# Kernel optimization log

Hardware: AMD Instinct MI355X
Metric: run time of the kernel (lower is better)

## Reference

```python
import jax, jax.numpy as jnp
import numpy as np

M, N, D = 16384, 16384, 256


def setup_inputs() -> dict:
    key = jax.random.key(0)
    k1, k2, k3 = jax.random.split(key, 3)
    x = jax.random.normal(k1, (M, D), dtype=jnp.float32)
    X = jax.random.normal(k2, (N, D), dtype=jnp.float32)
    residuals = jax.random.normal(k3, (N,), dtype=jnp.float32)
    return {"x": x, "X": X, "residuals": residuals}


def reference(x, X, residuals):
    n, d = X.shape
    # Scott's rule: h = mean(std(X, unbiased)) * n^(-1/(d+4))
    h = jnp.mean(jnp.std(X, axis=0, ddof=1)) * (n ** (-1.0 / (d + 4)))
    inv_bw_sq = 1.0 / (2.0 * h * h)
    sq = (jnp.sum(x * x, axis=1)[:, None]
          + jnp.sum(X * X, axis=1)[None, :]
          - 2.0 * (x @ X.T))
    sq = jnp.maximum(sq, 0.0)
    w = jnp.exp(-sq * inv_bw_sq)                     # (m, n)
    num = w @ residuals                              # (m,)
    den = jnp.sum(w, axis=1) + 1e-8                  # (m,)
    return num / den
```

## Files before the change

kernel.cpp:

```cpp
#include <hip/hip_runtime.h>
#include <stdint.h>

#define MDIM 16384
#define NDIM 16384
#define DDIM 256
#define NSPLIT 4
#define NSTRIP 4096
#define BM 128
#define NT 32

typedef __attribute__((ext_vector_type(16))) float f32x16;
typedef __attribute__((ext_vector_type(8))) int i32x8;

#define SC1 0x7F7F7F7F

static constexpr size_t COLPART_OFF = 0;
static constexpr size_t SCAL_OFF    = 512u * 1024u;
static constexpr size_t AX_OFF      = SCAL_OFF + 1024u;
static constexpr size_t BXR_OFF     = AX_OFF + 64u * 1024u;
static constexpr size_t BXM_OFF     = BXR_OFF + 64u * 1024u;
static constexpr size_t X8_OFF      = 1ull << 20;
static constexpr size_t B8_OFF      = X8_OFF + (4ull << 20);
static constexpr size_t NUMP_OFF    = B8_OFF + (4ull << 20) + (512ull << 10);
static constexpr size_t DENP_OFF    = NUMP_OFF + (size_t)NSPLIT * MDIM * 4u;

__device__ inline unsigned short f2bf_rne(float f) {
    uint32_t u = __builtin_bit_cast(uint32_t, f);
    u += 0x7fffu + ((u >> 16) & 1u);
    return (unsigned short)(u >> 16);
}

__global__ void k1_colstats(const float* __restrict__ X, float2* __restrict__ part) {
    const int l  = threadIdx.x & 63;
    const int wv = threadIdx.x >> 6;
    const int b  = blockIdx.x;
    const float* p = X + (size_t)(b * 256 + wv * 64) * DDIM + l * 4;
    float4 s = {0.f, 0.f, 0.f, 0.f}, q = {0.f, 0.f, 0.f, 0.f};
#pragma unroll 8
    for (int r = 0; r < 64; ++r) {
        float4 v = *(const float4*)(p + (size_t)r * DDIM);
        s.x += v.x; s.y += v.y; s.z += v.z; s.w += v.w;
        q.x += v.x * v.x; q.y += v.y * v.y; q.z += v.z * v.z; q.w += v.w * v.w;
    }
    __shared__ float4 sA[4][64], qA[4][64];
    sA[wv][l] = s; qA[wv][l] = q;
    __syncthreads();
    if (wv == 0) {
#pragma unroll
        for (int i = 1; i < 4; ++i) {
            float4 si = sA[i][l], qi = qA[i][l];
            s.x += si.x; s.y += si.y; s.z += si.z; s.w += si.w;
            q.x += qi.x; q.y += qi.y; q.z += qi.z; q.w += qi.w;
        }
        part[b * 256 + l * 4 + 0] = make_float2(s.x, q.x);
        part[b * 256 + l * 4 + 1] = make_float2(s.y, q.y);
        part[b * 256 + l * 4 + 2] = make_float2(s.z, q.z);
        part[b * 256 + l * 4 + 3] = make_float2(s.w, q.w);
    }
}

__global__ void k2_finalize(const float2* __restrict__ part, float* __restrict__ scal) {
    const int t = threadIdx.x;
    float s = 0.f, sq = 0.f;
#pragma unroll 8
    for (int b = 0; b < 64; ++b) {
        float2 v = part[b * 256 + t];
        s += v.x; sq += v.y;
    }
    const float n = (float)NDIM;
    float var = (sq - s * s / n) / (n - 1.0f);
    float sd  = sqrtf(fmaxf(var, 0.f));
    __shared__ float red[256];
    red[t] = sd;
    __syncthreads();
    for (int o = 128; o > 0; o >>= 1) {
        if (t < o) red[t] += red[t + o];
        __syncthreads();
    }
    if (t == 0) {
        float h = (red[0] / 256.0f) * exp2f(log2f(n) * (-1.0f / (DDIM + 4.0f)));
        float c = 1.0f / (2.0f * h * h);
        scal[0] = c;
        scal[1] = sqrtf(2.0f * c);
    }
}

__global__ void k3_prep(const float* __restrict__ x, const float* __restrict__ X,
                        unsigned char* __restrict__ x8T, unsigned char* __restrict__ B8T,
                        float* __restrict__ ax,
                        const float* __restrict__ resid, unsigned int* __restrict__ bxrp,
                        unsigned int* __restrict__ bxminu,
                        const float* __restrict__ scal) {
    const int l    = threadIdx.x & 63;
    const int wv   = threadIdx.x >> 6;
    const bool isB = blockIdx.x >= (MDIM / 16);
    const int row  = (blockIdx.x - (isB ? MDIM / 16 : 0)) * 16 + wv * 4 + (l >> 4);
    const int q    = l & 15;
    const float* src = isB ? X : x;
    const float c = scal[0], s = scal[1];

    float4 v[4];
    const float* pr = src + (size_t)row * DDIM + q * 16;
#pragma unroll
    for (int i = 0; i < 4; ++i) v[i] = *(const float4*)(pr + i * 4);

    float nsq = 0.f;
#pragma unroll
    for (int i = 0; i < 4; ++i)
        nsq += v[i].x * v[i].x + v[i].y * v[i].y + v[i].z * v[i].z + v[i].w * v[i].w;
#pragma unroll
    for (int o = 1; o < 16; o <<= 1) nsq += __shfl_xor(nsq, o);

    uint4 u;
    {
        unsigned int t0 = 0, t1 = 0, t2 = 0, t3 = 0;
        t0 = __builtin_amdgcn_cvt_pk_fp8_f32(v[0].x * s, v[0].y * s, t0, 0);
        t0 = __builtin_amdgcn_cvt_pk_fp8_f32(v[0].z * s, v[0].w * s, t0, 1);
        t1 = __builtin_amdgcn_cvt_pk_fp8_f32(v[1].x * s, v[1].y * s, t1, 0);
        t1 = __builtin_amdgcn_cvt_pk_fp8_f32(v[1].z * s, v[1].w * s, t1, 1);
        t2 = __builtin_amdgcn_cvt_pk_fp8_f32(v[2].x * s, v[2].y * s, t2, 0);
        t2 = __builtin_amdgcn_cvt_pk_fp8_f32(v[2].z * s, v[2].w * s, t2, 1);
        t3 = __builtin_amdgcn_cvt_pk_fp8_f32(v[3].x * s, v[3].y * s, t3, 0);
        t3 = __builtin_amdgcn_cvt_pk_fp8_f32(v[3].z * s, v[3].w * s, t3, 1);
        u = make_uint4(t0, t1, t2, t3);
    }

    const int ks64 = q >> 2, lh = (q >> 1) & 1, eh = q & 1;
    if (isB) {
        const size_t off = (size_t)(row >> 6) * 16384 + ks64 * 4096 + ((row >> 5) & 1) * 2048
                         + lh * 1024 + (row & 31) * 32 + eh * 16;
        *(uint4*)(B8T + off) = u;
        if (q == 0) {
            bxrp[row] = ((unsigned int)f2bf_rne(resid[row]) << 16) | f2bf_rne(-c * nsq);
            atomicMin(&bxminu[row >> 6], __builtin_bit_cast(unsigned int, nsq));
        }
    } else {
        const size_t off = (size_t)(row >> 7) * 32768 + ks64 * 8192 + ((row >> 5) & 3) * 2048
                         + lh * 1024 + (row & 31) * 32 + eh * 16;
        *(uint4*)(x8T + off) = u;
        if (q == 0) ax[row] = -c * nsq;
    }
}

__global__ __launch_bounds__(256, 2)
void k4_main(const unsigned char* __restrict__ x8T, const unsigned char* __restrict__ B8T,
             const float* __restrict__ ax, const unsigned int* __restrict__ bxrp,
             const unsigned int* __restrict__ bxminu, const float* __restrict__ scal,
             float* __restrict__ nump, float* __restrict__ denp) {
    __shared__ float ldsBxm[NSTRIP / 64];
    __shared__ float ldsAcc[2 * BM];

    const int tid  = threadIdx.x;
    const int lane = tid & 63;
    const int wv   = tid >> 6;
    const int wr   = wv >> 1;
    const int wc   = wv & 1;
    const int l31  = lane & 31;
    const int lhi  = lane >> 5;

    const int f  = blockIdx.x;
    const int sw = (f & 7) * 64 + (f >> 3);
    const int mt = sw & 127;
    const int by = sw >> 7;
    const int m0 = mt * BM;
    const int n0 = by * NSTRIP;

    const float c = scal[0];
    if (tid < NSTRIP / 64)
        ldsBxm[tid] = -c * __builtin_bit_cast(float, bxminu[(n0 >> 6) + tid]);
    ldsAcc[tid] = 0.f;

    float axm = fmaxf(ax[m0 + lane], ax[m0 + 64 + lane]);
#pragma unroll
    for (int o = 1; o < 64; o <<= 1) axm = fmaxf(axm, __shfl_xor(axm, o));

    const unsigned char* Ab = x8T + (size_t)mt * 32768 + lhi * 1024 + l31 * 32;
    i32x8 aF[2][4];
#pragma unroll
    for (int rf = 0; rf < 2; ++rf)
#pragma unroll
        for (int ks = 0; ks < 4; ++ks)
            aF[rf][ks] = *(const i32x8*)(Ab + ks * 8192 + (wr * 2 + rf) * 2048);

    const unsigned char* Bb = B8T + (size_t)n0 * 256 + (size_t)wc * 16384 + lhi * 1024 + l31 * 32;
    i32x8 bF[4][2];
#pragma unroll
    for (int s = 0; s < 2; ++s) {
        bF[s][0] = *(const i32x8*)(Bb + s * 4096);
        bF[s][1] = *(const i32x8*)(Bb + s * 4096 + 2048);
    }

    __syncthreads();

    if ((f >> 8) & 1) __builtin_amdgcn_s_sleep(4);

    f32x16 acc[2][2];

#pragma unroll 1
    for (int nt = 0; nt < NT; ++nt) {
#pragma unroll
        for (int ks = 0; ks < 4; ++ks) {
            {
                const int sp = nt * 4 + ks + 2;
                const size_t off = (size_t)(sp >> 2) * 32768 + (size_t)(sp & 3) * 4096;
                bF[(ks + 2) & 3][0] = *(const i32x8*)(Bb + off);
                bF[(ks + 2) & 3][1] = *(const i32x8*)(Bb + off + 2048);
            }
            __builtin_amdgcn_sched_barrier(0);
            __builtin_amdgcn_s_setprio(1);
#pragma unroll
            for (int rf = 0; rf < 2; ++rf)
#pragma unroll
                for (int cf = 0; cf < 2; ++cf) {
                    if (ks == 0)
                        acc[rf][cf] = __builtin_amdgcn_mfma_scale_f32_32x32x64_f8f6f4(
                            aF[rf][ks], bF[ks & 3][cf], (f32x16)(0.f), 0, 0, 0, SC1, 0, SC1);
                    else
                        acc[rf][cf] = __builtin_amdgcn_mfma_scale_f32_32x32x64_f8f6f4(
                            aF[rf][ks], bF[ks & 3][cf], acc[rf][cf], 0, 0, 0, SC1, 0, SC1);
                }
            __builtin_amdgcn_s_setprio(0);
            __builtin_amdgcn_sched_barrier(0);

            if (ks == 3) {
                const float bxm = ldsBxm[nt * 2 + wc];
                float m = -1e30f;
#pragma unroll
                for (int i = 0; i < 2; ++i)
#pragma unroll
                    for (int j = 0; j < 2; ++j)
#pragma unroll
                        for (int r = 0; r < 16; r += 4) {
                            f32x16 v = acc[i][j];
                            m = fmaxf(m, fmaxf(fmaxf(v[r], v[r + 1]), fmaxf(v[r + 2], v[r + 3])));
                        }
                if (!__all(m + axm + bxm < -104.0f)) {
                    float bxv[2], rv[2];
#pragma unroll
                    for (int cf = 0; cf < 2; ++cf) {
                        unsigned int pk = bxrp[n0 + nt * 128 + wc * 64 + cf * 32 + l31];
                        bxv[cf] = __builtin_bit_cast(float, pk << 16);
                        rv[cf]  = __builtin_bit_cast(float, pk & 0xffff0000u);
                    }
#pragma unroll
                    for (int rf = 0; rf < 2; ++rf)
#pragma unroll
                        for (int r = 0; r < 16; ++r) {
                            const int row = wr * 64 + rf * 32 + (r & 3) + 8 * (r >> 2) + 4 * lhi;
                            const float axv = ax[m0 + row];
                            float nv = 0.f, dv = 0.f;
#pragma unroll
                            for (int cf = 0; cf < 2; ++cf) {
                                const float arg = fminf(acc[rf][cf][r] + axv + bxv[cf], 0.f);
                                const float w = expf(arg);
                                nv = fmaf(w, rv[cf], nv);
                                dv += w;
                            }
#pragma unroll
                            for (int o = 1; o < 32; o <<= 1) { nv += __shfl_xor(nv, o); dv += __shfl_xor(dv, o); }
                            if (l31 == 0) {
                                atomicAdd(&ldsAcc[row * 2 + 0], nv);
                                atomicAdd(&ldsAcc[row * 2 + 1], dv);
                            }
                        }
                }
            }
        }
    }

    __syncthreads();
    if (tid < BM) {
        nump[by * MDIM + m0 + tid] = ldsAcc[tid * 2 + 0];
        denp[by * MDIM + m0 + tid] = ldsAcc[tid * 2 + 1];
    }
}

__global__ void k5_div(const float* __restrict__ nump, const float* __restrict__ denp,
                       float* __restrict__ out) {
    const int i = blockIdx.x * 256 + threadIdx.x;
    float n = 0.f, d = 0.f;
#pragma unroll
    for (int s = 0; s < NSPLIT; ++s) { n += nump[s * MDIM + i]; d += denp[s * MDIM + i]; }
    out[i] = n / (d + 1e-8f);
}

extern "C" void kernel_launch(void* const* d_in, const int* in_sizes, int n_in,
                              void* d_out, int out_size, void* d_ws, size_t ws_size,
                              hipStream_t stream) {
    const float* x     = (const float*)d_in[0];
    const float* X     = (const float*)d_in[1];
    const float* resid = (const float*)d_in[2];
    float* out = (float*)d_out;

    char* w = (char*)d_ws;
    float2* colpart      = (float2*)(w + COLPART_OFF);
    float*  scal         = (float*)(w + SCAL_OFF);
    float*  ax           = (float*)(w + AX_OFF);
    unsigned int* bxrp   = (unsigned int*)(w + BXR_OFF);
    unsigned int* bxminu = (unsigned int*)(w + BXM_OFF);
    unsigned char* x8    = (unsigned char*)(w + X8_OFF);
    unsigned char* B8    = (unsigned char*)(w + B8_OFF);
    float* nump          = (float*)(w + NUMP_OFF);
    float* denp          = (float*)(w + DENP_OFF);

    k1_colstats<<<64, 256, 0, stream>>>(X, colpart);
    k2_finalize<<<1, 256, 0, stream>>>(colpart, scal);
    k3_prep<<<(MDIM + NDIM) / 16, 256, 0, stream>>>(x, X, x8, B8, ax, resid, bxrp, bxminu, scal);
    k4_main<<<512, 256, 0, stream>>>(x8, B8, ax, bxrp, bxminu, scal, nump, denp);
    k5_div<<<MDIM / 256, 256, 0, stream>>>(nump, denp, out);
}
```

Before: 95.77 us.

## Stage B tiles through LDS with async global_load_lds instead of per-wave register loads

Changes the B8 packing layout to 16-byte rows and streams B fragments into a 4-slot LDS ring buffer with direct global-to-LDS loads. The waves now share one copy of each B tile instead of each wave loading its own fragments into registers. Synchronisation uses explicit vmcnt waits and a workgroup barrier every k-step, and the staggered s_sleep is removed. This is meant to cut redundant global traffic and register pressure, but it adds a barrier per MFMA group plus LDS read latency.

```diff
diff --git a/kernel.cpp b/kernel.cpp
--- a/kernel.cpp
+++ b/kernel.cpp
@@ -11,6 +11,7 @@
 
 typedef __attribute__((ext_vector_type(16))) float f32x16;
 typedef __attribute__((ext_vector_type(8))) int i32x8;
+typedef __attribute__((ext_vector_type(4))) int i32x4;
 
 #define SC1 0x7F7F7F7F
 
@@ -28,6 +29,11 @@
     uint32_t u = __builtin_bit_cast(uint32_t, f);
     u += 0x7fffu + ((u >> 16) & 1u);
     return (unsigned short)(u >> 16);
+}
+
+__device__ inline void gload16(const void* g, void* l) {
+    __builtin_amdgcn_global_load_lds((const __attribute__((address_space(1))) void*)g,
+                                     (__attribute__((address_space(3))) void*)l, 16, 0, 0);
 }
 
 __global__ void k1_colstats(const float* __restrict__ X, float2* __restrict__ part) {
@@ -127,8 +133,8 @@
 
     const int ks64 = q >> 2, lh = (q >> 1) & 1, eh = q & 1;
     if (isB) {
-        const size_t off = (size_t)(row >> 6) * 16384 + ks64 * 4096 + ((row >> 5) & 1) * 2048
-                         + lh * 1024 + (row & 31) * 32 + eh * 16;
+        const size_t off = (size_t)(row >> 6) * 16384 + ks64 * 4096 + eh * 2048
+                         + lh * 1024 + (row & 63) * 16;
         *(uint4*)(B8T + off) = u;
         if (q == 0) {
             bxrp[row] = ((unsigned int)f2bf_rne(resid[row]) << 16) | f2bf_rne(-c * nsq);
@@ -147,6 +153,7 @@
              const float* __restrict__ ax, const unsigned int* __restrict__ bxrp,
              const unsigned int* __restrict__ bxminu, const float* __restrict__ scal,
              float* __restrict__ nump, float* __restrict__ denp) {
+    __shared__ unsigned char ldsB[4 * 8192];
     __shared__ float ldsBxm[NSTRIP / 64];
     __shared__ float ldsAcc[2 * BM];
 
@@ -166,13 +173,8 @@
     const int n0 = by * NSTRIP;
 
     const float c = scal[0];
-    if (tid < NSTRIP / 64)
-        ldsBxm[tid] = -c * __builtin_bit_cast(float, bxminu[(n0 >> 6) + tid]);
-    ldsAcc[tid] = 0.f;
-
-    float axm = fmaxf(ax[m0 + lane], ax[m0 + 64 + lane]);
-#pragma unroll
-    for (int o = 1; o < 64; o <<= 1) axm = fmaxf(axm, __shfl_xor(axm, o));
+    const float ax0 = ax[m0 + lane], ax1 = ax[m0 + 64 + lane];
+    const float bxmv = -c * __builtin_bit_cast(float, bxminu[(n0 >> 6) + lane]);
 
     const unsigned char* Ab = x8T + (size_t)mt * 32768 + lhi * 1024 + l31 * 32;
     i32x8 aF[2][4];
@@ -182,48 +184,70 @@
         for (int ks = 0; ks < 4; ++ks)
             aF[rf][ks] = *(const i32x8*)(Ab + ks * 8192 + (wr * 2 + rf) * 2048);
 
-    const unsigned char* Bb = B8T + (size_t)n0 * 256 + (size_t)wc * 16384 + lhi * 1024 + l31 * 32;
-    i32x8 bF[4][2];
-#pragma unroll
-    for (int s = 0; s < 2; ++s) {
-        bF[s][0] = *(const i32x8*)(Bb + s * 4096);
-        bF[s][1] = *(const i32x8*)(Bb + s * 4096 + 2048);
-    }
-
-    __syncthreads();
-
-    if ((f >> 8) & 1) __builtin_amdgcn_s_sleep(4);
+    if (wv == 0) ldsBxm[lane] = bxmv;
+    ldsAcc[tid] = 0.f;
+
+    float axm = fmaxf(ax0, ax1);
+#pragma unroll
+    for (int o = 1; o < 64; o <<= 1) axm = fmaxf(axm, __shfl_xor(axm, o));
+
+    asm volatile("s_waitcnt vmcnt(0) lgkmcnt(0)" ::: "memory");
+    __builtin_amdgcn_sched_barrier(0);
+    __builtin_amdgcn_s_barrier();
+
+    auto stage = [&](int step) {
+        const int t    = (step >> 2) & (NT - 1);
+        const int ks64 = step & 3;
+        const int slot = step & 3;
+        const unsigned char* src = B8T + (size_t)((n0 >> 6) + t * 2 + wc) * 16384
+                                 + ks64 * 4096 + wr * 1024 + lane * 16;
+        char* dst = (char*)ldsB + slot * 8192 + wc * 4096 + wr * 1024;
+        gload16(src, dst);
+        gload16(src + 2048, dst + 2048);
+    };
+    auto ldb = [&](int step, int cf) -> i32x8 {
+        const unsigned char* p = ldsB + (step & 3) * 8192 + wc * 4096
+                               + lhi * 1024 + (cf * 32 + l31) * 16;
+        i32x4 lo = *(const i32x4*)p;
+        i32x4 hi = *(const i32x4*)(p + 2048);
+        return (i32x8){lo[0], lo[1], lo[2], lo[3], hi[0], hi[1], hi[2], hi[3]};
+    };
+
+    stage(0); stage(1);
 
     f32x16 acc[2][2];
 
 #pragma unroll 1
-    for (int nt = 0; nt < NT; ++nt) {
+    for (int nt_ = 0; nt_ < NT; ++nt_) {
 #pragma unroll
         for (int ks = 0; ks < 4; ++ks) {
-            {
-                const int sp = nt * 4 + ks + 2;
-                const size_t off = (size_t)(sp >> 2) * 32768 + (size_t)(sp & 3) * 4096;
-                bF[(ks + 2) & 3][0] = *(const i32x8*)(Bb + off);
-                bF[(ks + 2) & 3][1] = *(const i32x8*)(Bb + off + 2048);
+            const int s = nt_ * 4 + ks;
+            stage(s + 2);
+            asm volatile("s_waitcnt vmcnt(4)" ::: "memory");
+            __builtin_amdgcn_sched_barrier(0);
+            __builtin_amdgcn_s_barrier();
+            i32x8 b0 = ldb(s, 0);
+            i32x8 b1 = ldb(s, 1);
+            __builtin_amdgcn_s_setprio(1);
+#pragma unroll
+            for (int rf = 0; rf < 2; ++rf) {
+                if (ks == 0) {
+                    acc[rf][0] = __builtin_amdgcn_mfma_scale_f32_32x32x64_f8f6f4(
+                        aF[rf][ks], b0, (f32x16)(0.f), 0, 0, 0, SC1, 0, SC1);
+                    acc[rf][1] = __builtin_amdgcn_mfma_scale_f32_32x32x64_f8f6f4(
+                        aF[rf][ks], b1, (f32x16)(0.f), 0, 0, 0, SC1, 0, SC1);
+                } else {
+                    acc[rf][0] = __builtin_amdgcn_mfma_scale_f32_32x32x64_f8f6f4(
+                        aF[rf][ks], b0, acc[rf][0], 0, 0, 0, SC1, 0, SC1);
+                    acc[rf][1] = __builtin_amdgcn_mfma_scale_f32_32x32x64_f8f6f4(
+                        aF[rf][ks], b1, acc[rf][1], 0, 0, 0, SC1, 0, SC1);
+                }
             }
-            __builtin_amdgcn_sched_barrier(0);
-            __builtin_amdgcn_s_setprio(1);
-#pragma unroll
-            for (int rf = 0; rf < 2; ++rf)
-#pragma unroll
-                for (int cf = 0; cf < 2; ++cf) {
-                    if (ks == 0)
-                        acc[rf][cf] = __builtin_amdgcn_mfma_scale_f32_32x32x64_f8f6f4(
-                            aF[rf][ks], bF[ks & 3][cf], (f32x16)(0.f), 0, 0, 0, SC1, 0, SC1);
-                    else
-                        acc[rf][cf] = __builtin_amdgcn_mfma_scale_f32_32x32x64_f8f6f4(
-                            aF[rf][ks], bF[ks & 3][cf], acc[rf][cf], 0, 0, 0, SC1, 0, SC1);
-                }
             __builtin_amdgcn_s_setprio(0);
             __builtin_amdgcn_sched_barrier(0);
 
             if (ks == 3) {
-                const float bxm = ldsBxm[nt * 2 + wc];
+                const float bxm = ldsBxm[nt_ * 2 + wc];
                 float m = -1e30f;
 #pragma unroll
                 for (int i = 0; i < 2; ++i)
@@ -238,7 +262,7 @@
                     float bxv[2], rv[2];
 #pragma unroll
                     for (int cf = 0; cf < 2; ++cf) {
-                        unsigned int pk = bxrp[n0 + nt * 128 + wc * 64 + cf * 32 + l31];
+                        unsigned int pk = bxrp[n0 + nt_ * 128 + wc * 64 + cf * 32 + l31];
                         bxv[cf] = __builtin_bit_cast(float, pk << 16);
                         rv[cf]  = __builtin_bit_cast(float, pk & 0xffff0000u);
                     }
@@ -263,11 +287,14 @@
                                 atomicAdd(&ldsAcc[row * 2 + 1], dv);
                             }
                         }
+                    asm volatile("s_waitcnt vmcnt(0)" ::: "memory");
                 }
             }
         }
     }
 
+    asm volatile("s_waitcnt vmcnt(0) lgkmcnt(0)" ::: "memory");
+    __builtin_amdgcn_sched_barrier(0);
     __syncthreads();
     if (tid < BM) {
         nump[by * MDIM + m0 + tid] = ldsAcc[tid * 2 + 0];
```

After: 100.5 us. 1.05x slower.

## Quantize operands to FP4 e2m1 and use FP4 scaled MFMA

Applied to the files above, without the earlier changes.

Switches the packed x and X operands from FP8 to FP4 (e2m1) with a custom threshold quantizer. Memory layouts are repacked at half the bytes, and the scaled MFMA is run in FP4 mode with the upper half of each operand register zeroed. This halves operand bandwidth and may raise MFMA throughput, at a large accuracy cost for the distance computation inside an exponential. It also drops the staggered s_sleep for half of the blocks.

```diff
diff --git a/kernel.cpp b/kernel.cpp
--- a/kernel.cpp
+++ b/kernel.cpp
@@ -11,6 +11,7 @@
 
 typedef __attribute__((ext_vector_type(16))) float f32x16;
 typedef __attribute__((ext_vector_type(8))) int i32x8;
+typedef __attribute__((ext_vector_type(4))) int i32x4;
 
 #define SC1 0x7F7F7F7F
 
@@ -28,6 +29,14 @@
     uint32_t u = __builtin_bit_cast(uint32_t, f);
     u += 0x7fffu + ((u >> 16) & 1u);
     return (unsigned short)(u >> 16);
+}
+
+__device__ inline unsigned e2m1q(float v) {
+    const float a = __builtin_fabsf(v);
+    unsigned m = (unsigned)(a >= 0.25f) + (unsigned)(a >= 0.75f) + (unsigned)(a >= 1.25f)
+               + (unsigned)(a >= 1.75f) + (unsigned)(a >= 2.5f)  + (unsigned)(a >= 3.5f)
+               + (unsigned)(a >= 5.0f);
+    return m | ((__builtin_bit_cast(unsigned, v) >> 28) & 8u);
 }
 
 __global__ void k1_colstats(const float* __restrict__ X, float2* __restrict__ part) {
@@ -111,33 +120,31 @@
 #pragma unroll
     for (int o = 1; o < 16; o <<= 1) nsq += __shfl_xor(nsq, o);
 
-    uint4 u;
-    {
-        unsigned int t0 = 0, t1 = 0, t2 = 0, t3 = 0;
-        t0 = __builtin_amdgcn_cvt_pk_fp8_f32(v[0].x * s, v[0].y * s, t0, 0);
-        t0 = __builtin_amdgcn_cvt_pk_fp8_f32(v[0].z * s, v[0].w * s, t0, 1);
-        t1 = __builtin_amdgcn_cvt_pk_fp8_f32(v[1].x * s, v[1].y * s, t1, 0);
-        t1 = __builtin_amdgcn_cvt_pk_fp8_f32(v[1].z * s, v[1].w * s, t1, 1);
-        t2 = __builtin_amdgcn_cvt_pk_fp8_f32(v[2].x * s, v[2].y * s, t2, 0);
-        t2 = __builtin_amdgcn_cvt_pk_fp8_f32(v[2].z * s, v[2].w * s, t2, 1);
-        t3 = __builtin_amdgcn_cvt_pk_fp8_f32(v[3].x * s, v[3].y * s, t3, 0);
-        t3 = __builtin_amdgcn_cvt_pk_fp8_f32(v[3].z * s, v[3].w * s, t3, 1);
-        u = make_uint4(t0, t1, t2, t3);
-    }
-
-    const int ks64 = q >> 2, lh = (q >> 1) & 1, eh = q & 1;
+    float vs[16] = {v[0].x * s, v[0].y * s, v[0].z * s, v[0].w * s,
+                    v[1].x * s, v[1].y * s, v[1].z * s, v[1].w * s,
+                    v[2].x * s, v[2].y * s, v[2].z * s, v[2].w * s,
+                    v[3].x * s, v[3].y * s, v[3].z * s, v[3].w * s};
+    unsigned w0 = 0, w1 = 0;
+#pragma unroll
+    for (int i = 0; i < 4; ++i) {
+        w0 |= (e2m1q(vs[2 * i]) | (e2m1q(vs[2 * i + 1]) << 4)) << (8 * i);
+        w1 |= (e2m1q(vs[8 + 2 * i]) | (e2m1q(vs[9 + 2 * i]) << 4)) << (8 * i);
+    }
+    const uint2 u = make_uint2(w0, w1);
+
+    const int ks64 = q >> 2, lh = (q >> 1) & 1, eb = q & 1;
     if (isB) {
-        const size_t off = (size_t)(row >> 6) * 16384 + ks64 * 4096 + ((row >> 5) & 1) * 2048
-                         + lh * 1024 + (row & 31) * 32 + eh * 16;
-        *(uint4*)(B8T + off) = u;
+        const size_t off = (size_t)(row >> 6) * 8192 + ks64 * 2048 + lh * 1024
+                         + (row & 63) * 16 + eb * 8;
+        *(uint2*)(B8T + off) = u;
         if (q == 0) {
             bxrp[row] = ((unsigned int)f2bf_rne(resid[row]) << 16) | f2bf_rne(-c * nsq);
             atomicMin(&bxminu[row >> 6], __builtin_bit_cast(unsigned int, nsq));
         }
     } else {
-        const size_t off = (size_t)(row >> 7) * 32768 + ks64 * 8192 + ((row >> 5) & 3) * 2048
-                         + lh * 1024 + (row & 31) * 32 + eh * 16;
-        *(uint4*)(x8T + off) = u;
+        const size_t off = (size_t)(row >> 7) * 16384 + ks64 * 4096 + ((row >> 5) & 3) * 1024
+                         + lh * 512 + (row & 31) * 16 + eb * 8;
+        *(uint2*)(x8T + off) = u;
         if (q == 0) ax[row] = -c * nsq;
     }
 }
@@ -174,25 +181,28 @@
 #pragma unroll
     for (int o = 1; o < 64; o <<= 1) axm = fmaxf(axm, __shfl_xor(axm, o));
 
-    const unsigned char* Ab = x8T + (size_t)mt * 32768 + lhi * 1024 + l31 * 32;
+    const unsigned char* Ab = x8T + (size_t)mt * 16384 + lhi * 512 + l31 * 16;
     i32x8 aF[2][4];
 #pragma unroll
     for (int rf = 0; rf < 2; ++rf)
 #pragma unroll
-        for (int ks = 0; ks < 4; ++ks)
-            aF[rf][ks] = *(const i32x8*)(Ab + ks * 8192 + (wr * 2 + rf) * 2048);
-
-    const unsigned char* Bb = B8T + (size_t)n0 * 256 + (size_t)wc * 16384 + lhi * 1024 + l31 * 32;
+        for (int ks = 0; ks < 4; ++ks) {
+            i32x4 lo = *(const i32x4*)(Ab + ks * 4096 + (wr * 2 + rf) * 1024);
+            aF[rf][ks] = (i32x8){lo[0], lo[1], lo[2], lo[3], 0, 0, 0, 0};
+        }
+
+    const unsigned char* Bb = B8T + (size_t)((n0 >> 6) + wc) * 8192 + lhi * 1024 + l31 * 16;
     i32x8 bF[4][2];
 #pragma unroll
     for (int s = 0; s < 2; ++s) {
-        bF[s][0] = *(const i32x8*)(Bb + s * 4096);
-        bF[s][1] = *(const i32x8*)(Bb + s * 4096 + 2048);
+        const size_t off = (size_t)(s & 3) * 2048;
+        i32x4 b0 = *(const i32x4*)(Bb + off);
+        i32x4 b1 = *(const i32x4*)(Bb + off + 512);
+        bF[s][0] = (i32x8){b0[0], b0[1], b0[2], b0[3], 0, 0, 0, 0};
+        bF[s][1] = (i32x8){b1[0], b1[1], b1[2], b1[3], 0, 0, 0, 0};
     }
 
     __syncthreads();
-
-    if ((f >> 8) & 1) __builtin_amdgcn_s_sleep(4);
 
     f32x16 acc[2][2];
 
@@ -202,9 +212,11 @@
         for (int ks = 0; ks < 4; ++ks) {
             {
                 const int sp = nt * 4 + ks + 2;
-                const size_t off = (size_t)(sp >> 2) * 32768 + (size_t)(sp & 3) * 4096;
-                bF[(ks + 2) & 3][0] = *(const i32x8*)(Bb + off);
-                bF[(ks + 2) & 3][1] = *(const i32x8*)(Bb + off + 2048);
+                const size_t off = (size_t)(sp >> 2) * 16384 + (size_t)(sp & 3) * 2048;
+                i32x4 b0 = *(const i32x4*)(Bb + off);
+                i32x4 b1 = *(const i32x4*)(Bb + off + 512);
+                bF[(ks + 2) & 3][0] = (i32x8){b0[0], b0[1], b0[2], b0[3], 0, 0, 0, 0};
+                bF[(ks + 2) & 3][1] = (i32x8){b1[0], b1[1], b1[2], b1[3], 0, 0, 0, 0};
             }
             __builtin_amdgcn_sched_barrier(0);
             __builtin_amdgcn_s_setprio(1);
@@ -214,10 +226,10 @@
                 for (int cf = 0; cf < 2; ++cf) {
                     if (ks == 0)
                         acc[rf][cf] = __builtin_amdgcn_mfma_scale_f32_32x32x64_f8f6f4(
-                            aF[rf][ks], bF[ks & 3][cf], (f32x16)(0.f), 0, 0, 0, SC1, 0, SC1);
+                            aF[rf][ks], bF[ks & 3][cf], (f32x16)(0.f), 4, 4, 0, SC1, 0, SC1);
                     else
                         acc[rf][cf] = __builtin_amdgcn_mfma_scale_f32_32x32x64_f8f6f4(
-                            aF[rf][ks], bF[ks & 3][cf], acc[rf][cf], 0, 0, 0, SC1, 0, SC1);
+                            aF[rf][ks], bF[ks & 3][cf], acc[rf][cf], 4, 4, 0, SC1, 0, SC1);
                 }
             __builtin_amdgcn_s_setprio(0);
             __builtin_amdgcn_sched_barrier(0);
```

New measurement: 78.53 us. -18.0%, faster.
